# Kernel tuning notes

Measured on AMD Instinct MI355X. Metric: run time of the kernel, lower is better.

## Reference

```python
import jax, jax.numpy as jnp
import numpy as np

IN_SIZE = 2048 + 1  # features + scalar reward, per RolloutEncoder.__init__
HIDDEN = 1024       # config['rollout_enc_size']
T = 8192            # rollout buffer length


def setup_inputs() -> dict:
    key = jax.random.key(0)
    k1, k2, k3, k4, k5, k6 = jax.random.split(key, 6)
    s = 1.0 / np.sqrt(HIDDEN)  # torch GRUCell init scale
    return {
        "features": jax.random.normal(k1, (T, 2048), dtype=jnp.float32),
        "rewards": jax.random.normal(k2, (T,), dtype=jnp.float32),
        "w_ih": jax.random.uniform(k3, (3 * HIDDEN, IN_SIZE), jnp.float32, -s, s),
        "w_hh": jax.random.uniform(k4, (3 * HIDDEN, HIDDEN), jnp.float32, -s, s),
        "b_ih": jax.random.uniform(k5, (3 * HIDDEN,), jnp.float32, -s, s),
        "b_hh": jax.random.uniform(k6, (3 * HIDDEN,), jnp.float32, -s, s),
    }


def reference(features, rewards, w_ih, w_hh, b_ih, b_hh):
    H = w_hh.shape[1]
    # concat features with reward -> [T, 2049], matching torch.cat((features, reward.unsqueeze(0)), dim=1)
    x = jnp.concatenate([features, rewards[:, None]], axis=1)
    # precompute all input-side gate pre-activations in one big GEMM: [T, 3H]
    gi = x @ w_ih.T + b_ih
    gi_r, gi_z, gi_n = jnp.split(gi, 3, axis=1)

    w_hr, w_hz, w_hn = jnp.split(w_hh, 3, axis=0)
    b_hr, b_hz, b_hn = jnp.split(b_hh, 3)

    def step(h, g):  # h: [H]
        gr, gz, gn = g
        r = jax.nn.sigmoid(gr + h @ w_hr.T + b_hr)
        z = jax.nn.sigmoid(gz + h @ w_hz.T + b_hz)
        n = jnp.tanh(gn + r * (h @ w_hn.T + b_hn))
        h_new = (1.0 - z) * n + z * h
        return h_new, None

    h0 = jnp.zeros((H,), dtype=features.dtype)
    # dream_buffer.pop() consumes the LAST transition first -> reverse scan
    h_final, _ = jax.lax.scan(step, h0, (gi_r, gi_z, gi_n), reverse=True)
    return h_final[None, :]  # [1, H] like torch hidden
```

## Files before the change

### kernel.cpp

```cpp
#include <hip/hip_runtime.h>
#include <stdint.h>

#define T_STEPS 8192
#define HID     1024
#define IN_F    2048
#define N3H     3072
#define NREP    8

__global__ void init_pairs(unsigned int* pairs) {
    int i = blockIdx.x * blockDim.x + threadIdx.x;
    if (i < 2 * NREP * HID) pairs[i] = 0u;
}

__device__ __forceinline__ uint4 load_x4_scoped(const unsigned int* p) {
    uint4 r;
    asm volatile("global_load_dwordx4 %0, %1, off sc0 sc1\n\t"
                 "s_waitcnt vmcnt(0)"
                 : "=v"(r) : "v"(p) : "memory");
    return r;
}
__device__ __forceinline__ void store_scoped(unsigned int* p, unsigned int v) {
    asm volatile("global_store_dword %0, %1, off sc0 sc1"
                 :: "v"(p), "v"(v) : "memory");
}
__device__ __forceinline__ int tag_ok(const uint4& v, unsigned int w) {
    return (((v.x & 3u) == w) & ((v.y & 3u) == w) &
            ((v.z & 3u) == w) & ((v.w & 3u) == w));
}

#define GBM 64
#define GBN 64
#define GBK 32

__global__ __launch_bounds__(256) void gi_gemm(
    const float* __restrict__ feat,
    const float* __restrict__ rew,
    const float* __restrict__ w_ih,
    const float* __restrict__ b_ih,
    float* __restrict__ gi)
{
    __shared__ float As[GBK][GBM + 4];
    __shared__ float Bs[GBK][GBN + 4];

    const int tid = threadIdx.x;
    const int n0 = blockIdx.x * GBN;
    const int t0 = blockIdx.y * GBM;
    const int tx = tid & 15, ty = tid >> 4;
    const int lr = tid >> 3;
    const int lc = (tid & 7) * 4;

    float acc[4][4] = {{0.f}};

    for (int k0 = 0; k0 < IN_F; k0 += GBK) {
#pragma unroll
        for (int hh = 0; hh < 2; hh++) {
            const int r = lr + 32 * hh;
            const float4 a = *(const float4*)(feat + (size_t)(t0 + r) * IN_F + k0 + lc);
            As[lc + 0][r] = a.x; As[lc + 1][r] = a.y;
            As[lc + 2][r] = a.z; As[lc + 3][r] = a.w;
            const float* brow = w_ih + (size_t)(n0 + r) * (IN_F + 1) + k0 + lc;
            Bs[lc + 0][r] = brow[0]; Bs[lc + 1][r] = brow[1];
            Bs[lc + 2][r] = brow[2]; Bs[lc + 3][r] = brow[3];
        }
        __syncthreads();
#pragma unroll
        for (int kk = 0; kk < GBK; kk++) {
            const float4 a = *(const float4*)&As[kk][ty * 4];
            const float4 b = *(const float4*)&Bs[kk][tx * 4];
            acc[0][0] += a.x * b.x; acc[0][1] += a.x * b.y; acc[0][2] += a.x * b.z; acc[0][3] += a.x * b.w;
            acc[1][0] += a.y * b.x; acc[1][1] += a.y * b.y; acc[1][2] += a.y * b.z; acc[1][3] += a.y * b.w;
            acc[2][0] += a.z * b.x; acc[2][1] += a.z * b.y; acc[2][2] += a.z * b.z; acc[2][3] += a.z * b.w;
            acc[3][0] += a.w * b.x; acc[3][1] += a.w * b.y; acc[3][2] += a.w * b.z; acc[3][3] += a.w * b.w;
        }
        __syncthreads();
    }

    const int m = t0 + ty * 4;
    const int n = n0 + tx * 4;
    float wlast[4], bi[4];
#pragma unroll
    for (int c = 0; c < 4; c++) {
        wlast[c] = w_ih[(size_t)(n + c) * (IN_F + 1) + IN_F];
        bi[c]    = b_ih[n + c];
    }
#pragma unroll
    for (int r = 0; r < 4; r++) {
        const float rwv = rew[m + r];
        float4 v;
        v.x = acc[r][0] + rwv * wlast[0] + bi[0];
        v.y = acc[r][1] + rwv * wlast[1] + bi[1];
        v.z = acc[r][2] + rwv * wlast[2] + bi[2];
        v.w = acc[r][3] + rwv * wlast[3] + bi[3];
        *(float4*)(gi + (size_t)(m + r) * N3H + n) = v;
    }
}

__global__ __launch_bounds__(256, 2) void gru_scan(
    const float* __restrict__ gi,
    const float* __restrict__ w_hh,
    const float* __restrict__ b_hh,
    unsigned int* pairs,
    float* __restrict__ out)
{
    __shared__ float4 w_lds[3][4][HID / 4];
    __shared__ float4 h_lds[2][HID / 4];

    const int tid  = threadIdx.x;
    const int g    = blockIdx.x;
    const int j0   = g * 4;
    const int wave = tid >> 6;
    const int lane = tid & 63;
    const int myj  = j0 + wave;
    const int rep  = g & (NREP - 1);

#pragma unroll
    for (int r = 0; r < 12; r++) {
        const int gate = r >> 2, jl = r & 3;
        const float4* src = (const float4*)(w_hh + (size_t)(gate * HID + j0 + jl) * HID);
        w_lds[gate][jl][tid] = src[tid];
    }
    float b_r = 0.f, b_z = 0.f, b_n = 0.f;
    if (lane == 0) {
        b_r = b_hh[myj];
        b_z = b_hh[HID + myj];
        b_n = b_hh[2 * HID + myj];
    }
    __syncthreads();

    for (int i = 0; i < T_STEPS; i++) {
        const int t = T_STEPS - 1 - i;
        const unsigned int want = (unsigned int)(i & 3);
        const unsigned int* rbuf =
            pairs + ((size_t)(i & 1) * NREP + rep) * HID + tid * 4;

        float gi_r = 0.f, gi_z = 0.f, gi_n = 0.f;
        if (lane == 0) {
            const float* girow = gi + (size_t)t * N3H;
            gi_r = girow[myj];
            gi_z = girow[HID + myj];
            gi_n = girow[2 * HID + myj];
        }

        uint4 v;
        for (;;) {
            v = load_x4_scoped(rbuf);
            if (__all(tag_ok(v, want))) break;
        }

        float4 hv;
        hv.x = __uint_as_float(v.x);
        hv.y = __uint_as_float(v.y);
        hv.z = __uint_as_float(v.z);
        hv.w = __uint_as_float(v.w);
        h_lds[i & 1][tid] = hv;
        __syncthreads();

        float ar = 0.f, az = 0.f, an = 0.f;
        const float4* hb = h_lds[i & 1];
        const float4* wr = w_lds[0][wave];
        const float4* wz = w_lds[1][wave];
        const float4* wn = w_lds[2][wave];
#pragma unroll
        for (int m4 = 0; m4 < 4; m4++) {
            const int idx = lane + 64 * m4;
            const float4 h4 = hb[idx];
            const float4 r4 = wr[idx];
            const float4 z4 = wz[idx];
            const float4 n4 = wn[idx];
            ar += h4.x * r4.x + h4.y * r4.y + h4.z * r4.z + h4.w * r4.w;
            az += h4.x * z4.x + h4.y * z4.y + h4.z * z4.z + h4.w * z4.w;
            an += h4.x * n4.x + h4.y * n4.y + h4.z * n4.z + h4.w * n4.w;
        }
#pragma unroll
        for (int off = 32; off > 0; off >>= 1) {
            ar += __shfl_down(ar, off);
            az += __shfl_down(az, off);
            an += __shfl_down(an, off);
        }

        if (lane == 0) {
            const float hjold = ((const float*)h_lds[i & 1])[myj];
            const float r = 1.f / (1.f + __expf(-(gi_r + ar + b_r)));
            const float z = 1.f / (1.f + __expf(-(gi_z + az + b_z)));
            const float n = tanhf(gi_n + r * (an + b_n));
            const float hnew = (1.f - z) * n + z * hjold;
            if (i == T_STEPS - 1) {
                out[myj] = hnew;
            } else {
                unsigned int* sbase =
                    pairs + (size_t)((i + 1) & 1) * NREP * HID + myj;
                const unsigned int pk =
                    (__float_as_uint(hnew) & ~3u) | (unsigned int)((i + 1) & 3);
#pragma unroll
                for (int rr = 0; rr < NREP; rr++)
                    store_scoped(sbase + rr * HID, pk);
            }
        }
    }
}

extern "C" void kernel_launch(void* const* d_in, const int* in_sizes, int n_in,
                              void* d_out, int out_size, void* d_ws, size_t ws_size,
                              hipStream_t stream) {
    const float* feat = (const float*)d_in[0];
    const float* rew  = (const float*)d_in[1];
    const float* w_ih = (const float*)d_in[2];
    const float* w_hh = (const float*)d_in[3];
    const float* b_ih = (const float*)d_in[4];
    const float* b_hh = (const float*)d_in[5];
    float* out = (float*)d_out;

    float* gi = (float*)d_ws;
    unsigned int* pairs =
        (unsigned int*)((char*)d_ws + (size_t)T_STEPS * N3H * sizeof(float));

    hipLaunchKernelGGL(init_pairs, dim3((2 * NREP * HID + 255) / 256), dim3(256), 0, stream, pairs);
    hipLaunchKernelGGL(gi_gemm, dim3(N3H / GBN, T_STEPS / GBM), dim3(256), 0, stream,
                       feat, rew, w_ih, b_ih, gi);
    hipLaunchKernelGGL(gru_scan, dim3(256), dim3(256), 0, stream,
                       gi, w_hh, b_hh, pairs, out);
}
```

Measured before the change: 18.30 ms.

## Make each GRU scan wave independent with register-resident weights and wave-level polling

The scan kernel no longer stages w_hh and h in LDS. Each wave keeps its 3×1024 weight row slice in registers and polls the whole 1024-element hidden vector directly from the replicated global buffers, using four batched scoped loads. This removes the per-step __syncthreads and LDS round trip, so every wave advances on its own rather than waiting for the slowest wave in its block. The wave also keeps its own h value in a register, and the eight replica stores are spread across lanes. In exchange, each wave issues four times as much polling traffic per step, and the larger register footprint drops the occupancy hint to one block per SIMD group.

```diff
diff --git a/kernel.cpp b/kernel.cpp
--- a/kernel.cpp
+++ b/kernel.cpp
@@ -12,20 +12,40 @@
     if (i < 2 * NREP * HID) pairs[i] = 0u;
 }
 
-__device__ __forceinline__ uint4 load_x4_scoped(const unsigned int* p) {
-    uint4 r;
-    asm volatile("global_load_dwordx4 %0, %1, off sc0 sc1\n\t"
-                 "s_waitcnt vmcnt(0)"
-                 : "=v"(r) : "v"(p) : "memory");
-    return r;
+__device__ __forceinline__ void probe4(uint4& r0, uint4& r1, uint4& r2, uint4& r3,
+                                       const unsigned int* p0, const unsigned int* p1,
+                                       const unsigned int* p2, const unsigned int* p3) {
+    asm volatile(
+        "global_load_dwordx4 %0, %4, off sc0 sc1\n\t"
+        "global_load_dwordx4 %1, %5, off sc0 sc1\n\t"
+        "global_load_dwordx4 %2, %6, off sc0 sc1\n\t"
+        "global_load_dwordx4 %3, %7, off sc0 sc1\n\t"
+        "s_waitcnt vmcnt(0)"
+        : "=&v"(r0), "=&v"(r1), "=&v"(r2), "=&v"(r3)
+        : "v"(p0), "v"(p1), "v"(p2), "v"(p3)
+        : "memory");
 }
 __device__ __forceinline__ void store_scoped(unsigned int* p, unsigned int v) {
     asm volatile("global_store_dword %0, %1, off sc0 sc1"
                  :: "v"(p), "v"(v) : "memory");
 }
-__device__ __forceinline__ int tag_ok(const uint4& v, unsigned int w) {
-    return (((v.x & 3u) == w) & ((v.y & 3u) == w) &
-            ((v.z & 3u) == w) & ((v.w & 3u) == w));
+__device__ __forceinline__ int tag16_ok(const uint4& a, const uint4& b,
+                                        const uint4& c, const uint4& d,
+                                        unsigned int w) {
+    unsigned int x = (a.x ^ w) | (a.y ^ w) | (a.z ^ w) | (a.w ^ w)
+                   | (b.x ^ w) | (b.y ^ w) | (b.z ^ w) | (b.w ^ w)
+                   | (c.x ^ w) | (c.y ^ w) | (c.z ^ w) | (c.w ^ w)
+                   | (d.x ^ w) | (d.y ^ w) | (d.z ^ w) | (d.w ^ w);
+    return (x & 3u) == 0u;
+}
+__device__ __forceinline__ float dot4(const float4& a, const float4& b) {
+    return a.x * b.x + a.y * b.y + a.z * b.z + a.w * b.w;
+}
+__device__ __forceinline__ float4 u4_as_f4(const uint4& u) {
+    float4 f;
+    f.x = __uint_as_float(u.x); f.y = __uint_as_float(u.y);
+    f.z = __uint_as_float(u.z); f.w = __uint_as_float(u.w);
+    return f;
 }
 
 #define GBM 64
@@ -95,106 +115,87 @@
     }
 }
 
-__global__ __launch_bounds__(256, 2) void gru_scan(
+__global__ __launch_bounds__(256, 1) void gru_scan(
     const float* __restrict__ gi,
     const float* __restrict__ w_hh,
     const float* __restrict__ b_hh,
     unsigned int* pairs,
     float* __restrict__ out)
 {
-    __shared__ float4 w_lds[3][4][HID / 4];
-    __shared__ float4 h_lds[2][HID / 4];
-
     const int tid  = threadIdx.x;
     const int g    = blockIdx.x;
-    const int j0   = g * 4;
     const int wave = tid >> 6;
     const int lane = tid & 63;
-    const int myj  = j0 + wave;
-    const int rep  = g & (NREP - 1);
-
-#pragma unroll
-    for (int r = 0; r < 12; r++) {
-        const int gate = r >> 2, jl = r & 3;
-        const float4* src = (const float4*)(w_hh + (size_t)(gate * HID + j0 + jl) * HID);
-        w_lds[gate][jl][tid] = src[tid];
-    }
-    float b_r = 0.f, b_z = 0.f, b_n = 0.f;
-    if (lane == 0) {
-        b_r = b_hh[myj];
-        b_z = b_hh[HID + myj];
-        b_n = b_hh[2 * HID + myj];
-    }
-    __syncthreads();
-
-    for (int i = 0; i < T_STEPS; i++) {
+    const int j    = g * 4 + wave;
+    const int rep  = j & (NREP - 1);
+
+    float4 wreg[3][4];
+#pragma unroll
+    for (int gate = 0; gate < 3; ++gate)
+#pragma unroll
+        for (int c = 0; c < 4; ++c)
+            wreg[gate][c] = *(const float4*)(
+                w_hh + (size_t)(gate * HID + j) * HID + c * 256 + 4 * lane);
+
+    const float b_r = b_hh[j];
+    const float b_z = b_hh[HID + j];
+    const float b_n = b_hh[2 * HID + j];
+
+    float hj = 0.f;
+
+    for (int i = 0; i < T_STEPS; ++i) {
         const int t = T_STEPS - 1 - i;
         const unsigned int want = (unsigned int)(i & 3);
         const unsigned int* rbuf =
-            pairs + ((size_t)(i & 1) * NREP + rep) * HID + tid * 4;
-
-        float gi_r = 0.f, gi_z = 0.f, gi_n = 0.f;
-        if (lane == 0) {
-            const float* girow = gi + (size_t)t * N3H;
-            gi_r = girow[myj];
-            gi_z = girow[HID + myj];
-            gi_n = girow[2 * HID + myj];
-        }
-
-        uint4 v;
+            pairs + ((size_t)(i & 1) * NREP + rep) * HID;
+        const unsigned int* p0 = rbuf +   0 + 4 * lane;
+        const unsigned int* p1 = rbuf + 256 + 4 * lane;
+        const unsigned int* p2 = rbuf + 512 + 4 * lane;
+        const unsigned int* p3 = rbuf + 768 + 4 * lane;
+
+        const float* girow = gi + (size_t)t * N3H + j;
+        const float gi_r = girow[0];
+        const float gi_z = girow[HID];
+        const float gi_n = girow[2 * HID];
+
+        uint4 r0, r1, r2, r3;
         for (;;) {
-            v = load_x4_scoped(rbuf);
-            if (__all(tag_ok(v, want))) break;
-        }
-
-        float4 hv;
-        hv.x = __uint_as_float(v.x);
-        hv.y = __uint_as_float(v.y);
-        hv.z = __uint_as_float(v.z);
-        hv.w = __uint_as_float(v.w);
-        h_lds[i & 1][tid] = hv;
-        __syncthreads();
-
-        float ar = 0.f, az = 0.f, an = 0.f;
-        const float4* hb = h_lds[i & 1];
-        const float4* wr = w_lds[0][wave];
-        const float4* wz = w_lds[1][wave];
-        const float4* wn = w_lds[2][wave];
-#pragma unroll
-        for (int m4 = 0; m4 < 4; m4++) {
-            const int idx = lane + 64 * m4;
-            const float4 h4 = hb[idx];
-            const float4 r4 = wr[idx];
-            const float4 z4 = wz[idx];
-            const float4 n4 = wn[idx];
-            ar += h4.x * r4.x + h4.y * r4.y + h4.z * r4.z + h4.w * r4.w;
-            az += h4.x * z4.x + h4.y * z4.y + h4.z * z4.z + h4.w * z4.w;
-            an += h4.x * n4.x + h4.y * n4.y + h4.z * n4.z + h4.w * n4.w;
+            probe4(r0, r1, r2, r3, p0, p1, p2, p3);
+            if (__all(tag16_ok(r0, r1, r2, r3, want))) break;
+        }
+
+        float ar, az, an;
+        {
+            const float4 h0 = u4_as_f4(r0);
+            ar  = dot4(h0, wreg[0][0]); az  = dot4(h0, wreg[1][0]); an  = dot4(h0, wreg[2][0]);
+            const float4 h1 = u4_as_f4(r1);
+            ar += dot4(h1, wreg[0][1]); az += dot4(h1, wreg[1][1]); an += dot4(h1, wreg[2][1]);
+            const float4 h2 = u4_as_f4(r2);
+            ar += dot4(h2, wreg[0][2]); az += dot4(h2, wreg[1][2]); an += dot4(h2, wreg[2][2]);
+            const float4 h3 = u4_as_f4(r3);
+            ar += dot4(h3, wreg[0][3]); az += dot4(h3, wreg[1][3]); an += dot4(h3, wreg[2][3]);
         }
 #pragma unroll
         for (int off = 32; off > 0; off >>= 1) {
-            ar += __shfl_down(ar, off);
-            az += __shfl_down(az, off);
-            an += __shfl_down(an, off);
-        }
-
-        if (lane == 0) {
-            const float hjold = ((const float*)h_lds[i & 1])[myj];
-            const float r = 1.f / (1.f + __expf(-(gi_r + ar + b_r)));
-            const float z = 1.f / (1.f + __expf(-(gi_z + az + b_z)));
-            const float n = tanhf(gi_n + r * (an + b_n));
-            const float hnew = (1.f - z) * n + z * hjold;
-            if (i == T_STEPS - 1) {
-                out[myj] = hnew;
-            } else {
-                unsigned int* sbase =
-                    pairs + (size_t)((i + 1) & 1) * NREP * HID + myj;
-                const unsigned int pk =
-                    (__float_as_uint(hnew) & ~3u) | (unsigned int)((i + 1) & 3);
-#pragma unroll
-                for (int rr = 0; rr < NREP; rr++)
-                    store_scoped(sbase + rr * HID, pk);
-            }
+            ar += __shfl_xor(ar, off);
+            az += __shfl_xor(az, off);
+            an += __shfl_xor(an, off);
+        }
+
+        const float r = 1.f / (1.f + __expf(-(gi_r + ar + b_r)));
+        const float z = 1.f / (1.f + __expf(-(gi_z + az + b_z)));
+        const float n = tanhf(gi_n + r * (an + b_n));
+        const float hnew = (1.f - z) * n + z * hj;
+        hj = hnew;
+
+        if (i == T_STEPS - 1) {
+            if (lane == 0) out[j] = hnew;
+        } else {
+            const unsigned int pk =
+                (__float_as_uint(hnew) & ~3u) | (unsigned int)((i + 1) & 3);
+            unsigned int* sbase =
+                pairs + (size_t)((i + 1) & 1) * NREP * HID + j;
+            if (lane < NREP) store_scoped(sbase + lane * HID, pk);
         }
     }
 }
```

Result: slower. 50.91 ms (+178.2%).

## Relay hidden state through per-XCD L2 buffers via elected relay block

Applied to the files above, without the earlier changes.

Replaces the 8-way replicated system-scope broadcast of the hidden state with a single home buffer. One elected block per XCD polls the home buffer at device (LLC) scope and copies it into an XCD-local exchange buffer. The other blocks on that XCD poll that buffer with L2-scope loads, and fall back to polling the home buffer if the relay does not show up within a bounded number of tries. Each lane now keeps its own h_j in a register, and all lanes compute the gate math through an xor-shuffle reduction. This is meant to cut cross-die coherence traffic and writer-side stores on the serial critical path, at the cost of an extra relay hop, a reliance on XCC_ID and co-residency, and possible hangs or stale reads if L2 scoping behaves unexpectedly.

```diff
diff --git a/kernel.cpp b/kernel.cpp
--- a/kernel.cpp
+++ b/kernel.cpp
@@ -5,19 +5,30 @@
 #define HID     1024
 #define IN_F    2048
 #define N3H     3072
-#define NREP    8
-
-__global__ void init_pairs(unsigned int* pairs) {
+#define NXCD    8
+
+__global__ void init_exchange(unsigned int* p, int n) {
     int i = blockIdx.x * blockDim.x + threadIdx.x;
-    if (i < 2 * NREP * HID) pairs[i] = 0u;
-}
-
-__device__ __forceinline__ uint4 load_x4_scoped(const unsigned int* p) {
+    if (i < n) p[i] = 0u;
+}
+
+__device__ __forceinline__ uint4 probe_llc(const unsigned int* p) {
     uint4 r;
     asm volatile("global_load_dwordx4 %0, %1, off sc0 sc1\n\t"
                  "s_waitcnt vmcnt(0)"
                  : "=v"(r) : "v"(p) : "memory");
     return r;
+}
+__device__ __forceinline__ uint4 probe_l2(const unsigned int* p) {
+    uint4 r;
+    asm volatile("global_load_dwordx4 %0, %1, off sc0\n\t"
+                 "s_waitcnt vmcnt(0)"
+                 : "=v"(r) : "v"(p) : "memory");
+    return r;
+}
+__device__ __forceinline__ void store_l2(unsigned int* p, unsigned int v) {
+    asm volatile("global_store_dword %0, %1, off sc0"
+                 :: "v"(p), "v"(v) : "memory");
 }
 __device__ __forceinline__ void store_scoped(unsigned int* p, unsigned int v) {
     asm volatile("global_store_dword %0, %1, off sc0 sc1"
@@ -99,52 +110,93 @@
     const float* __restrict__ gi,
     const float* __restrict__ w_hh,
     const float* __restrict__ b_hh,
-    unsigned int* pairs,
+    unsigned int* home,
+    unsigned int* xbuf,
+    unsigned int* claim,
     float* __restrict__ out)
 {
     __shared__ float4 w_lds[3][4][HID / 4];
     __shared__ float4 h_lds[2][HID / 4];
+    __shared__ unsigned int s_flags;
 
     const int tid  = threadIdx.x;
     const int g    = blockIdx.x;
-    const int j0   = g * 4;
     const int wave = tid >> 6;
     const int lane = tid & 63;
-    const int myj  = j0 + wave;
-    const int rep  = g & (NREP - 1);
+    const int myj  = g * 4 + wave;
+
+    unsigned int xcd;
+    asm volatile("s_getreg_b32 %0, hwreg(HW_REG_XCC_ID)" : "=s"(xcd));
+    xcd &= (NXCD - 1);
+
+    if (tid == 0) {
+        unsigned int old = atomicCAS(&claim[xcd], 0u, 1u + (unsigned int)g);
+        s_flags = (old == 0u ? 1u : 0u) | (xcd << 8);
+    }
 
 #pragma unroll
     for (int r = 0; r < 12; r++) {
         const int gate = r >> 2, jl = r & 3;
-        const float4* src = (const float4*)(w_hh + (size_t)(gate * HID + j0 + jl) * HID);
+        const float4* src = (const float4*)(w_hh + (size_t)(gate * HID + g * 4 + jl) * HID);
         w_lds[gate][jl][tid] = src[tid];
     }
-    float b_r = 0.f, b_z = 0.f, b_n = 0.f;
-    if (lane == 0) {
-        b_r = b_hh[myj];
-        b_z = b_hh[HID + myj];
-        b_n = b_hh[2 * HID + myj];
-    }
+    const float b_r = b_hh[myj];
+    const float b_z = b_hh[HID + myj];
+    const float b_n = b_hh[2 * HID + myj];
     __syncthreads();
+
+    const bool is_relay = (s_flags & 1u) != 0u;
+    const unsigned int myx = (s_flags >> 8) & (NXCD - 1);
+
+    bool local_ok = false;
+    bool use_home = false;
+    float hj = 0.f;
 
     for (int i = 0; i < T_STEPS; i++) {
         const int t = T_STEPS - 1 - i;
         const unsigned int want = (unsigned int)(i & 3);
-        const unsigned int* rbuf =
-            pairs + ((size_t)(i & 1) * NREP + rep) * HID + tid * 4;
-
-        float gi_r = 0.f, gi_z = 0.f, gi_n = 0.f;
-        if (lane == 0) {
-            const float* girow = gi + (size_t)t * N3H;
-            gi_r = girow[myj];
-            gi_z = girow[HID + myj];
-            gi_n = girow[2 * HID + myj];
-        }
+        const unsigned int* hb = home + (size_t)(i & 1) * HID + tid * 4;
+        unsigned int* xb = xbuf + ((size_t)myx * 2 + (size_t)(i & 1)) * HID + tid * 4;
+
+        const float* girow = gi + (size_t)t * N3H + myj;
+        const float gi_r = girow[0];
+        const float gi_z = girow[HID];
+        const float gi_n = girow[2 * HID];
 
         uint4 v;
-        for (;;) {
-            v = load_x4_scoped(rbuf);
-            if (__all(tag_ok(v, want))) break;
+        if (is_relay) {
+            for (;;) {
+                v = probe_llc(hb);
+                if (__all(tag_ok(v, want))) break;
+            }
+            store_l2(xb + 0, v.x);
+            store_l2(xb + 1, v.y);
+            store_l2(xb + 2, v.z);
+            store_l2(xb + 3, v.w);
+        } else if (!use_home) {
+            if (local_ok) {
+                for (;;) {
+                    v = probe_l2(xb);
+                    if (__all(tag_ok(v, want))) break;
+                }
+            } else {
+                int got = 0;
+                for (int tries = 0; tries < 4096; ++tries) {
+                    v = probe_l2(xb);
+                    if (__all(tag_ok(v, want))) { got = 1; break; }
+                }
+                if (got) {
+                    if (i >= 1) local_ok = true;
+                } else {
+                    use_home = true;
+                }
+            }
+        }
+        if (use_home && !is_relay) {
+            for (;;) {
+                v = probe_llc(hb);
+                if (__all(tag_ok(v, want))) break;
+            }
         }
 
         float4 hv;
@@ -156,14 +208,14 @@
         __syncthreads();
 
         float ar = 0.f, az = 0.f, an = 0.f;
-        const float4* hb = h_lds[i & 1];
+        const float4* hbuf = h_lds[i & 1];
         const float4* wr = w_lds[0][wave];
         const float4* wz = w_lds[1][wave];
         const float4* wn = w_lds[2][wave];
 #pragma unroll
         for (int m4 = 0; m4 < 4; m4++) {
             const int idx = lane + 64 * m4;
-            const float4 h4 = hb[idx];
+            const float4 h4 = hbuf[idx];
             const float4 r4 = wr[idx];
             const float4 z4 = wz[idx];
             const float4 n4 = wn[idx];
@@ -173,28 +225,24 @@
         }
 #pragma unroll
         for (int off = 32; off > 0; off >>= 1) {
-            ar += __shfl_down(ar, off);
-            az += __shfl_down(az, off);
-            an += __shfl_down(an, off);
-        }
-
-        if (lane == 0) {
-            const float hjold = ((const float*)h_lds[i & 1])[myj];
-            const float r = 1.f / (1.f + __expf(-(gi_r + ar + b_r)));
-            const float z = 1.f / (1.f + __expf(-(gi_z + az + b_z)));
-            const float n = tanhf(gi_n + r * (an + b_n));
-            const float hnew = (1.f - z) * n + z * hjold;
-            if (i == T_STEPS - 1) {
-                out[myj] = hnew;
-            } else {
-                unsigned int* sbase =
-                    pairs + (size_t)((i + 1) & 1) * NREP * HID + myj;
-                const unsigned int pk =
-                    (__float_as_uint(hnew) & ~3u) | (unsigned int)((i + 1) & 3);
-#pragma unroll
-                for (int rr = 0; rr < NREP; rr++)
-                    store_scoped(sbase + rr * HID, pk);
-            }
+            ar += __shfl_xor(ar, off);
+            az += __shfl_xor(az, off);
+            an += __shfl_xor(an, off);
+        }
+
+        const float r = 1.f / (1.f + __expf(-(gi_r + ar + b_r)));
+        const float z = 1.f / (1.f + __expf(-(gi_z + az + b_z)));
+        const float n = tanhf(gi_n + r * (an + b_n));
+        const float hnew = (1.f - z) * n + z * hj;
+        hj = hnew;
+
+        if (i == T_STEPS - 1) {
+            if (lane == 0) out[myj] = hnew;
+        } else {
+            const unsigned int pk =
+                (__float_as_uint(hnew) & ~3u) | (unsigned int)((i + 1) & 3);
+            if (lane == 0)
+                store_scoped(home + (size_t)((i + 1) & 1) * HID + myj, pk);
         }
     }
 }
@@ -211,12 +259,15 @@
     float* out = (float*)d_out;
 
     float* gi = (float*)d_ws;
-    unsigned int* pairs =
-        (unsigned int*)((char*)d_ws + (size_t)T_STEPS * N3H * sizeof(float));
-
-    hipLaunchKernelGGL(init_pairs, dim3((2 * NREP * HID + 255) / 256), dim3(256), 0, stream, pairs);
+    unsigned int* home  = (unsigned int*)((char*)d_ws + (size_t)T_STEPS * N3H * sizeof(float));
+    unsigned int* xbuf  = home + 2 * HID;
+    unsigned int* claim = xbuf + NXCD * 2 * HID;
+    const int n_zero = 2 * HID + NXCD * 2 * HID + NXCD;
+
+    hipLaunchKernelGGL(init_exchange, dim3((n_zero + 255) / 256), dim3(256), 0, stream,
+                       home, n_zero);
     hipLaunchKernelGGL(gi_gemm, dim3(N3H / GBN, T_STEPS / GBM), dim3(256), 0, stream,
                        feat, rew, w_ih, b_ih, gi);
     hipLaunchKernelGGL(gru_scan, dim3(256), dim3(256), 0, stream,
-                       gi, w_hh, b_hh, pairs, out);
-}
+                       gi, w_hh, b_hh, home, xbuf, claim, out);
+}
```

Measured after the change: 30.01 ms. +64.0%, slower.
